# Kernel tuning notes

Hardware: AMD Instinct MI355X
Metric: run time of the kernel (lower is better)

The kernel has to match this reference:

```python
import jax, jax.numpy as jnp
import numpy as np

L, D, H, E, K, HID = 4096, 1024, 16, 8, 2, 4096
HEAD_DIM = D // H
SCALE = 1.0 / np.sqrt(HEAD_DIM)


def setup_inputs() -> dict:
    key = jax.random.key(0)
    ks = jax.random.split(key, 9)
    s = 0.02
    return {
        "Q": jax.random.normal(ks[0], (L, D), dtype=jnp.float32),
        "K": jax.random.normal(ks[1], (L, D), dtype=jnp.float32),
        "V": jax.random.normal(ks[2], (L, D), dtype=jnp.float32),
        "gate_w": jax.random.normal(ks[3], (D, E), dtype=jnp.float32) * s,
        "w1": jax.random.normal(ks[4], (E, D, HID), dtype=jnp.float32) * s,
        "b1": jnp.zeros((E, HID), dtype=jnp.float32),
        "w2": jax.random.normal(ks[5], (E, HID, D), dtype=jnp.float32) * s,
        "b2": jnp.zeros((E, D), dtype=jnp.float32),
    }


def attention(Q, Kt, V):
    # [L, D] -> [L, H, head_dim]
    q = Q.reshape(L, H, HEAD_DIM)
    k = Kt.reshape(L, H, HEAD_DIM)
    v = V.reshape(L, H, HEAD_DIM)
    scores = jnp.einsum("qhd,khd->hqk", q, k) * SCALE  # [H, L, L]
    probs = jax.nn.softmax(scores, axis=-1)
    out = jnp.einsum("hqk,khd->qhd", probs, v)  # [L, H, head_dim]
    return out.reshape(L, D)


def moe(x, gate_w, w1, b1, w2, b2):
    # x: [N, D]; top-k gating with softmax over selected logits
    logits = x @ gate_w  # [N, E]
    topv, topi = jax.lax.top_k(logits, K)  # [N, K]
    topw = jax.nn.softmax(topv, axis=-1)
    rows = jnp.arange(x.shape[0])[:, None]
    full_w = jnp.zeros_like(logits).at[rows, topi].set(topw)  # [N, E]
    # dense-masked expert compute (mathematically identical: zero weights kill
    # unrouted tokens). GELU is exact (erf), matching torch nn.GELU default.
    h = jax.nn.gelu(jnp.einsum("nd,edh->enh", x, w1) + b1[:, None, :],
                    approximate=False)  # [E, N, HID]
    y = jnp.einsum("enh,ehd->end", h, w2) + b2[:, None, :]  # [E, N, D]
    return jnp.einsum("ne,end->nd", full_w, y)  # weighted combine


def reference(Q, K, V, gate_w, w1, b1, w2, b2):
    attn_out = attention(Q, K, V)              # [L, D]
    out = moe(attn_out, gate_w, w1, b1, w2, b2)  # [L, D]
    return out
```

## Files before the change

kernel.cpp:

```cpp
#include <hip/hip_runtime.h>
#include <hip/hip_bf16.h>
#include <math.h>

#define L_SEQ 4096
#define DMODEL 1024
#define NHEAD 16
#define HDIM 64
#define NEXP 8
#define NHID 4096
#define NSLOT (L_SEQ * 2)

typedef __attribute__((ext_vector_type(4))) float f32x4;
typedef __attribute__((ext_vector_type(8))) short s16x8;
typedef __attribute__((ext_vector_type(4))) short s16x4;

__device__ __forceinline__ short f2bf(float f) {
  __hip_bfloat16 h = __float2bfloat16(f);
  return *reinterpret_cast<short*>(&h);
}
__device__ __forceinline__ float bf2f(short s) {
  __hip_bfloat16 h;
  *reinterpret_cast<short*>(&h) = s;
  return __bfloat162float(h);
}
__device__ __forceinline__ void split3(float a, short& h, short& m, short& l) {
  h = f2bf(a);
  float r = a - bf2f(h);
  m = f2bf(r);
  float r2 = r - bf2f(m);
  l = f2bf(r2);
}
__device__ __forceinline__ void tsplit3(float a, short& h, short& m, short& l) {
  unsigned u = __float_as_uint(a);
  unsigned uh = u & 0xffff0000u;
  float fh = __uint_as_float(uh);
  float r1 = a - fh;
  unsigned um = __float_as_uint(r1) & 0xffff0000u;
  float fm = __uint_as_float(um);
  float r2 = r1 - fm;
  unsigned ul = __float_as_uint(r2) & 0xffff0000u;
  h = (short)(uh >> 16); m = (short)(um >> 16); l = (short)(ul >> 16);
}
__device__ __forceinline__ void gload16(const void* g, void* l) {
  __builtin_amdgcn_global_load_lds(
      (const __attribute__((address_space(1))) void*)g,
      (__attribute__((address_space(3))) void*)l, 16, 0, 0);
}

__global__ __launch_bounds__(256) void split_kernel(const float* __restrict__ src,
                                                    short* __restrict__ hs,
                                                    short* __restrict__ ms,
                                                    short* __restrict__ ls,
                                                    float scale, int nquad) {
  int i = blockIdx.x * 256 + threadIdx.x;
  for (; i < nquad; i += gridDim.x * 256) {
    f32x4 a = reinterpret_cast<const f32x4*>(src)[i];
    a *= scale;
    s16x4 h4, m4, l4;
    #pragma unroll
    for (int j = 0; j < 4; ++j) {
      short h, m, l;
      split3(a[j], h, m, l);
      h4[j] = h; m4[j] = m; l4[j] = l;
    }
    reinterpret_cast<s16x4*>(hs)[i] = h4;
    reinterpret_cast<s16x4*>(ms)[i] = m4;
    reinterpret_cast<s16x4*>(ls)[i] = l4;
  }
}

__global__ __launch_bounds__(256) void split_vt_kernel(const float* __restrict__ V,
                                                       short* __restrict__ Vth,
                                                       short* __restrict__ Vtm,
                                                       short* __restrict__ Vtl) {
  __shared__ float Vlds[64][65];
  const int k0 = blockIdx.x * 64;
  const int head = blockIdx.y;
  const int t = threadIdx.x;
  {
    int r = t >> 2, c = (t & 3) * 16;
    const f32x4* src = reinterpret_cast<const f32x4*>(&V[(size_t)(k0 + r) * DMODEL + head * HDIM + c]);
    #pragma unroll
    for (int j = 0; j < 4; ++j)
      *reinterpret_cast<f32x4*>(&Vlds[r][c + 4 * j]) = src[j];
  }
  __syncthreads();
  {
    int d = t >> 2, kc = (t & 3) * 16;
    s16x8 h8[2], m8[2], l8[2];
    #pragma unroll
    for (int j = 0; j < 16; ++j) {
      float v = Vlds[kc + j][d];
      short h, m, l;
      split3(v, h, m, l);
      h8[j >> 3][j & 7] = h; m8[j >> 3][j & 7] = m; l8[j >> 3][j & 7] = l;
    }
    size_t base = (size_t)(head * HDIM + d) * L_SEQ + k0 + kc;
    *reinterpret_cast<s16x8*>(&Vth[base]) = h8[0];
    *reinterpret_cast<s16x8*>(&Vth[base + 8]) = h8[1];
    *reinterpret_cast<s16x8*>(&Vtm[base]) = m8[0];
    *reinterpret_cast<s16x8*>(&Vtm[base + 8]) = m8[1];
    *reinterpret_cast<s16x8*>(&Vtl[base]) = l8[0];
    *reinterpret_cast<s16x8*>(&Vtl[base + 8]) = l8[1];
  }
}

__global__ __launch_bounds__(256) void wtrans_kernel(const float* __restrict__ src,
                                                     short* __restrict__ dst,
                                                     int R, int C) {
  __shared__ float T[64][65];
  const int e = blockIdx.z;
  const int r0 = blockIdx.y * 64, c0 = blockIdx.x * 64;
  const size_t sbase = (size_t)e * R * C;
  const int t = threadIdx.x;
  {
    int rr = t >> 2, cc = (t & 3) * 16;
    #pragma unroll
    for (int j = 0; j < 4; ++j)
      *reinterpret_cast<f32x4*>(&T[rr][cc + 4 * j]) =
          *reinterpret_cast<const f32x4*>(&src[sbase + (size_t)(r0 + rr) * C + c0 + cc + 4 * j]);
  }
  __syncthreads();
  {
    int c = t >> 2, r = (t & 3) * 16;
    s16x8 v0, v1;
    #pragma unroll
    for (int j = 0; j < 8; ++j) { v0[j] = f2bf(T[r + j][c]); v1[j] = f2bf(T[r + 8 + j][c]); }
    size_t dbase = ((size_t)e * C + c0 + c) * R + r0 + r;
    *reinterpret_cast<s16x8*>(&dst[dbase]) = v0;
    *reinterpret_cast<s16x8*>(&dst[dbase + 8]) = v1;
  }
}

__global__ __launch_bounds__(256) void attn_mfma(
    const short* __restrict__ Qh, const short* __restrict__ Qm, const short* __restrict__ Ql,
    const short* __restrict__ Kh, const short* __restrict__ Km, const short* __restrict__ Kl,
    const short* __restrict__ Vth, const short* __restrict__ Vtm, const short* __restrict__ Vtl,
    float* __restrict__ X) {
  __shared__ short Ks[3][64][68];
  __shared__ short Vs[3][64][68];
  __shared__ short Ps[4][3][16][68];
  const int lin = blockIdx.x;
  const int swz = (lin & 7) * 128 + (lin >> 3);
  const int head = swz >> 6;
  const int q0 = (swz & 63) << 6;
  const int t = threadIdx.x;
  const int lane = t & 63;
  const int wq = t >> 6;
  const int lq = lane & 15;
  const int lg = lane >> 4;

  const short* Qp[3] = {Qh, Qm, Ql};
  const short* Kp[3] = {Kh, Km, Kl};
  const short* Vp[3] = {Vth, Vtm, Vtl};

  s16x8 qf[3][2];
  {
    size_t qrow = (size_t)(q0 + wq * 16 + lq) * DMODEL + head * HDIM;
    #pragma unroll
    for (int s = 0; s < 3; ++s)
      #pragma unroll
      for (int dc = 0; dc < 2; ++dc)
        qf[s][dc] = *reinterpret_cast<const s16x8*>(&Qp[s][qrow + dc * 32 + lg * 8]);
  }

  s16x8 sK[3][2], sV[3][2];
  const int c0 = t * 2;
  const int row0 = c0 >> 3, ch0 = (c0 & 7) * 8;
  const int row1 = (c0 + 1) >> 3, ch1 = ((c0 + 1) & 7) * 8;

  #define LOAD_TILE(k0v)                                                                  \
    _Pragma("unroll")                                                                     \
    for (int s = 0; s < 3; ++s) {                                                         \
      sK[s][0] = *reinterpret_cast<const s16x8*>(&Kp[s][(size_t)((k0v) + row0) * DMODEL + head * HDIM + ch0]); \
      sK[s][1] = *reinterpret_cast<const s16x8*>(&Kp[s][(size_t)((k0v) + row1) * DMODEL + head * HDIM + ch1]); \
      sV[s][0] = *reinterpret_cast<const s16x8*>(&Vp[s][(size_t)(head * HDIM + row0) * L_SEQ + (k0v) + ch0]);  \
      sV[s][1] = *reinterpret_cast<const s16x8*>(&Vp[s][(size_t)(head * HDIM + row1) * L_SEQ + (k0v) + ch1]);  \
    }

  f32x4 acc[4];
  #pragma unroll
  for (int dt = 0; dt < 4; ++dt) acc[dt] = (f32x4)0.f;
  float l_run = 0.f;
  const float LOG2E = 1.4426950408889634f;
  const float MBIAS = 46.166241f;

  LOAD_TILE(0);

  for (int kt64 = 0; kt64 < 64; ++kt64) {
    __syncthreads();
    #pragma unroll
    for (int s = 0; s < 3; ++s) {
      *reinterpret_cast<s16x8*>(&Ks[s][row0][ch0]) = sK[s][0];
      *reinterpret_cast<s16x8*>(&Ks[s][row1][ch1]) = sK[s][1];
      *reinterpret_cast<s16x8*>(&Vs[s][row0][ch0]) = sV[s][0];
      *reinterpret_cast<s16x8*>(&Vs[s][row1][ch1]) = sV[s][1];
    }
    __syncthreads();
    if (kt64 < 63) { LOAD_TILE((kt64 + 1) * 64); }

    f32x4 st[4];
    #pragma unroll
    for (int kt = 0; kt < 4; ++kt) {
      st[kt] = (f32x4)0.f;
      #pragma unroll
      for (int dc = 0; dc < 2; ++dc) {
        s16x8 ah = *reinterpret_cast<const s16x8*>(&Ks[0][kt * 16 + lq][dc * 32 + lg * 8]);
        s16x8 am = *reinterpret_cast<const s16x8*>(&Ks[1][kt * 16 + lq][dc * 32 + lg * 8]);
        s16x8 al = *reinterpret_cast<const s16x8*>(&Ks[2][kt * 16 + lq][dc * 32 + lg * 8]);
        st[kt] = __builtin_amdgcn_mfma_f32_16x16x32_bf16(am, qf[1][dc], st[kt], 0, 0, 0);
        st[kt] = __builtin_amdgcn_mfma_f32_16x16x32_bf16(al, qf[0][dc], st[kt], 0, 0, 0);
        st[kt] = __builtin_amdgcn_mfma_f32_16x16x32_bf16(ah, qf[2][dc], st[kt], 0, 0, 0);
        st[kt] = __builtin_amdgcn_mfma_f32_16x16x32_bf16(am, qf[0][dc], st[kt], 0, 0, 0);
        st[kt] = __builtin_amdgcn_mfma_f32_16x16x32_bf16(ah, qf[1][dc], st[kt], 0, 0, 0);
        st[kt] = __builtin_amdgcn_mfma_f32_16x16x32_bf16(ah, qf[0][dc], st[kt], 0, 0, 0);
      }
    }

    float psum = 0.f;
    #pragma unroll
    for (int kt = 0; kt < 4; ++kt) {
      s16x4 h4, m4, l4;
      #pragma unroll
      for (int r = 0; r < 4; ++r) {
        float p = exp2f(fmaf(st[kt][r], LOG2E, -MBIAS));
        psum += p;
        short h, m, l;
        tsplit3(p, h, m, l);
        h4[r] = h; m4[r] = m; l4[r] = l;
      }
      int kcol = kt * 16 + lg * 4;
      *reinterpret_cast<s16x4*>(&Ps[wq][0][lq][kcol]) = h4;
      *reinterpret_cast<s16x4*>(&Ps[wq][1][lq][kcol]) = m4;
      *reinterpret_cast<s16x4*>(&Ps[wq][2][lq][kcol]) = l4;
    }
    psum += __shfl_xor(psum, 16);
    psum += __shfl_xor(psum, 32);
    l_run += psum;

    #pragma unroll
    for (int kc = 0; kc < 2; ++kc) {
      s16x8 ph = *reinterpret_cast<const s16x8*>(&Ps[wq][0][lq][kc * 32 + lg * 8]);
      s16x8 pm = *reinterpret_cast<const s16x8*>(&Ps[wq][1][lq][kc * 32 + lg * 8]);
      s16x8 pl = *reinterpret_cast<const s16x8*>(&Ps[wq][2][lq][kc * 32 + lg * 8]);
      #pragma unroll
      for (int dt = 0; dt < 4; ++dt) {
        s16x8 vh = *reinterpret_cast<const s16x8*>(&Vs[0][dt * 16 + lq][kc * 32 + lg * 8]);
        s16x8 vm = *reinterpret_cast<const s16x8*>(&Vs[1][dt * 16 + lq][kc * 32 + lg * 8]);
        s16x8 vl = *reinterpret_cast<const s16x8*>(&Vs[2][dt * 16 + lq][kc * 32 + lg * 8]);
        acc[dt] = __builtin_amdgcn_mfma_f32_16x16x32_bf16(pm, vm, acc[dt], 0, 0, 0);
        acc[dt] = __builtin_amdgcn_mfma_f32_16x16x32_bf16(pl, vh, acc[dt], 0, 0, 0);
        acc[dt] = __builtin_amdgcn_mfma_f32_16x16x32_bf16(ph, vl, acc[dt], 0, 0, 0);
        acc[dt] = __builtin_amdgcn_mfma_f32_16x16x32_bf16(pm, vh, acc[dt], 0, 0, 0);
        acc[dt] = __builtin_amdgcn_mfma_f32_16x16x32_bf16(ph, vm, acc[dt], 0, 0, 0);
        acc[dt] = __builtin_amdgcn_mfma_f32_16x16x32_bf16(ph, vh, acc[dt], 0, 0, 0);
      }
    }
  }

  float inv = 1.f / l_run;
  float inv_r[4];
  #pragma unroll
  for (int r = 0; r < 4; ++r) {
    int src = (lg * 4 + r) << 2;
    inv_r[r] = __int_as_float(__builtin_amdgcn_ds_bpermute(src, __float_as_int(inv)));
  }
  #pragma unroll
  for (int dt = 0; dt < 4; ++dt)
    #pragma unroll
    for (int r = 0; r < 4; ++r)
      X[(size_t)(q0 + wq * 16 + lg * 4 + r) * DMODEL + head * HDIM + dt * 16 + lq] = acc[dt][r] * inv_r[r];
}

__global__ __launch_bounds__(256) void tobf16_kernel(const float* __restrict__ src,
                                                     short* __restrict__ dst, int n8) {
  int i = blockIdx.x * 256 + threadIdx.x;
  if (i >= n8) return;
  const f32x4* s = reinterpret_cast<const f32x4*>(src) + (size_t)i * 2;
  f32x4 a = s[0], b = s[1];
  s16x8 r;
  #pragma unroll
  for (int j = 0; j < 4; ++j) { r[j] = f2bf(a[j]); r[4 + j] = f2bf(b[j]); }
  reinterpret_cast<s16x8*>(dst)[i] = r;
}

__global__ __launch_bounds__(256) void gate_kernel(const float* __restrict__ X,
                                                   const float* __restrict__ GW,
                                                   int* __restrict__ tokE,
                                                   float* __restrict__ tokW,
                                                   int* __restrict__ meta) {
  const int gid = blockIdx.x * 256 + threadIdx.x;
  const int n = gid >> 6;
  const int lane = threadIdx.x & 63;
  double lacc[8];
  #pragma unroll
  for (int e = 0; e < 8; ++e) lacc[e] = 0.0;
  #pragma unroll
  for (int ch = 0; ch < 4; ++ch) {
    int d0 = ch * 256 + lane * 4;
    f32x4 xv = *reinterpret_cast<const f32x4*>(&X[(size_t)n * DMODEL + d0]);
    #pragma unroll
    for (int j = 0; j < 4; ++j) {
      const f32x4* g = reinterpret_cast<const f32x4*>(&GW[(size_t)(d0 + j) * 8]);
      f32x4 g0 = g[0], g1 = g[1];
      double xd = (double)xv[j];
      lacc[0] += xd * (double)g0[0]; lacc[1] += xd * (double)g0[1];
      lacc[2] += xd * (double)g0[2]; lacc[3] += xd * (double)g0[3];
      lacc[4] += xd * (double)g1[0]; lacc[5] += xd * (double)g1[1];
      lacc[6] += xd * (double)g1[2]; lacc[7] += xd * (double)g1[3];
    }
  }
  #pragma unroll
  for (int e = 0; e < 8; ++e) {
    double v = lacc[e];
    #pragma unroll
    for (int off = 32; off > 0; off >>= 1) v += __shfl_down(v, off);
    lacc[e] = v;
  }
  if (lane == 0) {
    float lg[8];
    #pragma unroll
    for (int e = 0; e < 8; ++e) lg[e] = (float)lacc[e];
    int i0 = 0;
    for (int e = 1; e < 8; ++e) if (lg[e] > lg[i0]) i0 = e;
    int i1 = -1;
    for (int e = 0; e < 8; ++e) {
      if (e == i0) continue;
      if (i1 < 0 || lg[e] > lg[i1]) i1 = e;
    }
    float eb = expf(lg[i1] - lg[i0]);
    float wa = 1.f / (1.f + eb);
    float wb = eb * wa;
    tokE[2 * n] = i0; tokE[2 * n + 1] = i1;
    tokW[2 * n] = wa; tokW[2 * n + 1] = wb;
    atomicAdd(&meta[i0], 1);
    atomicAdd(&meta[i1], 1);
  }
}

__global__ void scan_kernel(int* meta) {
  if (threadIdx.x == 0) {
    int s = 0;
    for (int e = 0; e < 8; ++e) { meta[8 + e] = s; meta[16 + e] = s; s += meta[e]; }
  }
}

__global__ __launch_bounds__(256) void assign_kernel(const int* __restrict__ tokE,
                                                     const float* __restrict__ tokW,
                                                     int* __restrict__ meta,
                                                     int* __restrict__ list,
                                                     float* __restrict__ wl) {
  int n = blockIdx.x * 256 + threadIdx.x;
  if (n >= L_SEQ) return;
  #pragma unroll
  for (int k2 = 0; k2 < 2; ++k2) {
    int e = tokE[2 * n + k2];
    int slot = atomicAdd(&meta[16 + e], 1);
    list[slot] = n;
    wl[slot] = tokW[2 * n + k2];
  }
}

__global__ __launch_bounds__(256) void gemm1p_kernel(const short* __restrict__ Xb,
                                                     const short* __restrict__ W1t,
                                                     const float* __restrict__ B1,
                                                     const int* __restrict__ meta,
                                                     const int* __restrict__ list,
                                                     short* __restrict__ Hb) {
  const int e = blockIdx.z;
  const int cntE = meta[e];
  const int lin = blockIdx.x + gridDim.x * blockIdx.y;
  const int nwg = gridDim.x * gridDim.y;
  const int swz = (lin & 7) * (nwg >> 3) + (lin >> 3);
  const int m0 = (swz % gridDim.x) << 7;
  const int n0 = (swz / gridDim.x) << 7;
  if (m0 >= cntE) return;
  const int baseE = meta[8 + e];

  __shared__ short As[2][128 * 64];
  __shared__ short Bs[2][128 * 64];

  const int t = threadIdx.x;
  const int l = t & 63;
  const int w = t >> 6;
  const int wm = w >> 1, wn = w & 1;
  const int ln = l & 15, kg = l >> 4;

  size_t asrc[4], bsrc[4];
  #pragma unroll
  for (int c = 0; c < 4; ++c) {
    int row = c * 32 + w * 8 + (l >> 3);
    int idx = m0 + row; if (idx > cntE - 1) idx = cntE - 1;
    int grow = list[baseE + idx];
    int sch = (l & 7) ^ (row & 7);
    asrc[c] = ((size_t)grow * DMODEL + sch * 8) * 2;
    bsrc[c] = (((size_t)e * NHID + n0 + row) * DMODEL + sch * 8) * 2;
  }

  f32x4 acc[4][4];
  #pragma unroll
  for (int mi = 0; mi < 4; ++mi)
    #pragma unroll
    for (int ni = 0; ni < 4; ++ni) acc[mi][ni] = (f32x4)0.f;

  #define STAGE1(buf, ktv) do {                                                     \
    size_t koff = (size_t)(ktv) * 128;                                              \
    _Pragma("unroll")                                                               \
    for (int c = 0; c < 4; ++c) {                                                   \
      gload16((const char*)Xb + asrc[c] + koff, (char*)As + (buf) * 16384 + c * 4096 + w * 1024);  \
      gload16((const char*)W1t + bsrc[c] + koff, (char*)Bs + (buf) * 16384 + c * 4096 + w * 1024); \
    } } while (0)

  STAGE1(0, 0);
  __syncthreads();
  int cur = 0;
  for (int kt = 0; kt < 16; ++kt) {
    if (kt < 15) STAGE1(cur ^ 1, kt + 1);
    #pragma unroll
    for (int dc = 0; dc < 2; ++dc) {
      s16x8 af[4];
      #pragma unroll
      for (int mi = 0; mi < 4; ++mi) {
        int row = wm * 64 + mi * 16 + ln;
        int c = (dc * 4 + kg) ^ (row & 7);
        af[mi] = *reinterpret_cast<const s16x8*>((char*)As + cur * 16384 + row * 128 + c * 16);
      }
      #pragma unroll
      for (int ni = 0; ni < 4; ++ni) {
        int col = wn * 64 + ni * 16 + ln;
        int c = (dc * 4 + kg) ^ (col & 7);
        s16x8 bfr = *reinterpret_cast<const s16x8*>((char*)Bs + cur * 16384 + col * 128 + c * 16);
        #pragma unroll
        for (int mi = 0; mi < 4; ++mi)
          acc[mi][ni] = __builtin_amdgcn_mfma_f32_16x16x32_bf16(af[mi], bfr, acc[mi][ni], 0, 0, 0);
      }
    }
    __syncthreads();
    cur ^= 1;
  }

  #pragma unroll
  for (int mi = 0; mi < 4; ++mi) {
    #pragma unroll
    for (int r = 0; r < 4; ++r) {
      int rl = wm * 64 + mi * 16 + kg * 4 + r;
      if (m0 + rl >= cntE) continue;
      size_t hrow = (size_t)(baseE + m0 + rl) * NHID;
      #pragma unroll
      for (int ni = 0; ni < 4; ++ni) {
        int col = n0 + wn * 64 + ni * 16 + ln;
        float z = acc[mi][ni][r] + B1[e * NHID + col];
        float g = 0.5f * z * (1.f + erff(z * 0.70710678118f));
        Hb[hrow + col] = f2bf(g);
      }
    }
  }
}

__global__ __launch_bounds__(256) void gemm2p_kernel(const short* __restrict__ Hb,
                                                     const short* __restrict__ W2t,
                                                     const float* __restrict__ B2,
                                                     const int* __restrict__ meta,
                                                     const int* __restrict__ list,
                                                     const float* __restrict__ wl,
                                                     float* __restrict__ out) {
  const int e = blockIdx.z;
  const int cntE = meta[e];
  const int lin = blockIdx.x + gridDim.x * blockIdx.y;
  const int nwg = gridDim.x * gridDim.y;
  const int swz = (lin & 7) * (nwg >> 3) + (lin >> 3);
  const int m0 = (swz % gridDim.x) << 7;
  const int n0 = (swz / gridDim.x) << 7;
  if (m0 >= cntE) return;
  const int baseE = meta[8 + e];

  __shared__ short As[2][128 * 64];
  __shared__ short Bs[2][128 * 64];

  const int t = threadIdx.x;
  const int l = t & 63;
  const int w = t >> 6;
  const int wm = w >> 1, wn = w & 1;
  const int ln = l & 15, kg = l >> 4;

  size_t asrc[4], bsrc[4];
  #pragma unroll
  for (int c = 0; c < 4; ++c) {
    int row = c * 32 + w * 8 + (l >> 3);
    int idx = m0 + row; if (idx > cntE - 1) idx = cntE - 1;
    int sch = (l & 7) ^ (row & 7);
    asrc[c] = (((size_t)(baseE + idx)) * NHID + sch * 8) * 2;
    bsrc[c] = (((size_t)e * DMODEL + n0 + row) * NHID + sch * 8) * 2;
  }

  f32x4 acc[4][4];
  #pragma unroll
  for (int mi = 0; mi < 4; ++mi)
    #pragma unroll
    for (int ni = 0; ni < 4; ++ni) acc[mi][ni] = (f32x4)0.f;

  #define STAGE2(buf, ktv) do {                                                     \
    size_t koff = (size_t)(ktv) * 128;                                              \
    _Pragma("unroll")                                                               \
    for (int c = 0; c < 4; ++c) {                                                   \
      gload16((const char*)Hb + asrc[c] + koff, (char*)As + (buf) * 16384 + c * 4096 + w * 1024);  \
      gload16((const char*)W2t + bsrc[c] + koff, (char*)Bs + (buf) * 16384 + c * 4096 + w * 1024); \
    } } while (0)

  STAGE2(0, 0);
  __syncthreads();
  int cur = 0;
  for (int kt = 0; kt < 64; ++kt) {
    if (kt < 63) STAGE2(cur ^ 1, kt + 1);
    #pragma unroll
    for (int dc = 0; dc < 2; ++dc) {
      s16x8 af[4];
      #pragma unroll
      for (int mi = 0; mi < 4; ++mi) {
        int row = wm * 64 + mi * 16 + ln;
        int c = (dc * 4 + kg) ^ (row & 7);
        af[mi] = *reinterpret_cast<const s16x8*>((char*)As + cur * 16384 + row * 128 + c * 16);
      }
      #pragma unroll
      for (int ni = 0; ni < 4; ++ni) {
        int col = wn * 64 + ni * 16 + ln;
        int c = (dc * 4 + kg) ^ (col & 7);
        s16x8 bfr = *reinterpret_cast<const s16x8*>((char*)Bs + cur * 16384 + col * 128 + c * 16);
        #pragma unroll
        for (int mi = 0; mi < 4; ++mi)
          acc[mi][ni] = __builtin_amdgcn_mfma_f32_16x16x32_bf16(af[mi], bfr, acc[mi][ni], 0, 0, 0);
      }
    }
    __syncthreads();
    cur ^= 1;
  }

  #pragma unroll
  for (int mi = 0; mi < 4; ++mi) {
    #pragma unroll
    for (int r = 0; r < 4; ++r) {
      int rl = wm * 64 + mi * 16 + kg * 4 + r;
      if (m0 + rl >= cntE) continue;
      int slot = baseE + m0 + rl;
      int token = list[slot];
      float wgt = wl[slot];
      #pragma unroll
      for (int ni = 0; ni < 4; ++ni) {
        int col = n0 + wn * 64 + ni * 16 + ln;
        float z = acc[mi][ni][r] + B2[e * DMODEL + col];
        atomicAdd(&out[(size_t)token * DMODEL + col], wgt * z);
      }
    }
  }
}

extern "C" void kernel_launch(void* const* d_in, const int* in_sizes, int n_in,
                              void* d_out, int out_size, void* d_ws, size_t ws_size,
                              hipStream_t stream) {
  const float* Q  = (const float*)d_in[0];
  const float* K  = (const float*)d_in[1];
  const float* V  = (const float*)d_in[2];
  const float* GW = (const float*)d_in[3];
  const float* W1 = (const float*)d_in[4];
  const float* B1 = (const float*)d_in[5];
  const float* W2 = (const float*)d_in[6];
  const float* B2 = (const float*)d_in[7];
  float* out = (float*)d_out;

  const size_t SPLIT = (size_t)L_SEQ * DMODEL;
  const size_t WT_BYTES = (size_t)NEXP * NHID * DMODEL * 2;
  const size_t SPLIT_REGION = SPLIT * 2 * 9;
  const size_t SMALL = (size_t)L_SEQ * 2 * 4 * 2 + (size_t)NSLOT * 4 * 2 + 256;
  const size_t PRIMARY_BYTES = WT_BYTES * 2 + SPLIT_REGION + SPLIT * 4 + SMALL;
  if (ws_size < PRIMARY_BYTES) return;

  char* ws = (char*)d_ws;
  const int nquad = (int)(SPLIT / 4);

  size_t off = 0;
  short* W1t = (short*)(ws + off); off += WT_BYTES;
  short* W2t = (short*)(ws + off); off += WT_BYTES;
  char*  splits = ws + off;        off += SPLIT_REGION;
  short* Qh = (short*)(splits);
  short* Qm = Qh + SPLIT;  short* Ql = Qm + SPLIT;
  short* Kh = Ql + SPLIT;  short* Km = Kh + SPLIT;  short* Kl = Km + SPLIT;
  short* Vth = Kl + SPLIT; short* Vtm = Vth + SPLIT; short* Vtl = Vtm + SPLIT;
  short* Hb = (short*)splits;
  short* Xb = (short*)(splits + (size_t)NSLOT * NHID * 2);
  float* Xf = (float*)(ws + off);  off += SPLIT * 4;
  int*   tokE = (int*)(ws + off);  off += (size_t)L_SEQ * 2 * 4;
  float* tokW = (float*)(ws + off); off += (size_t)L_SEQ * 2 * 4;
  int*   list = (int*)(ws + off);  off += (size_t)NSLOT * 4;
  float* wl = (float*)(ws + off);  off += (size_t)NSLOT * 4;
  int*   meta = (int*)(ws + off);  off += 256;

  hipMemsetAsync(out, 0, (size_t)out_size * sizeof(float), stream);
  hipMemsetAsync(meta, 0, 256, stream);

  wtrans_kernel<<<dim3(64, 16, 8), 256, 0, stream>>>(W1, W1t, DMODEL, NHID);
  wtrans_kernel<<<dim3(16, 64, 8), 256, 0, stream>>>(W2, W2t, NHID, DMODEL);
  split_kernel<<<dim3(2048), 256, 0, stream>>>(Q, Qh, Qm, Ql, 0.125f, nquad);
  split_kernel<<<dim3(2048), 256, 0, stream>>>(K, Kh, Km, Kl, 1.0f, nquad);
  split_vt_kernel<<<dim3(64, 16), 256, 0, stream>>>(V, Vth, Vtm, Vtl);
  attn_mfma<<<dim3(1024), 256, 0, stream>>>(Qh, Qm, Ql, Kh, Km, Kl, Vth, Vtm, Vtl, Xf);
  tobf16_kernel<<<dim3(2048), 256, 0, stream>>>(Xf, Xb, (int)(SPLIT / 8));
  gate_kernel<<<dim3(1024), 256, 0, stream>>>(Xf, GW, tokE, tokW, meta);
  scan_kernel<<<1, 64, 0, stream>>>(meta);
  assign_kernel<<<dim3(16), 256, 0, stream>>>(tokE, tokW, meta, list, wl);
  gemm1p_kernel<<<dim3(32, 32, 8), 256, 0, stream>>>(Xb, W1t, B1, meta, list, Hb);
  gemm2p_kernel<<<dim3(32, 8, 8), 256, 0, stream>>>(Hb, W2t, B2, meta, list, wl, out);
}
```

Before: 1.099 ms.

## Deepen software pipelining in attention and MoE GEMM kernels

The attention kernel now uses 32-key tiles in double-buffered LDS, with register-staged prefetch two tiles ahead and compute interleaved between the two buffers. Both expert GEMM kernels move from a 2-stage 64-wide K pipeline to a 4-buffer 32-wide K pipeline that keeps three loads in flight, using explicit vmcnt waits and a single raw barrier per step. The aim is to hide global-load latency behind MFMA work and cut barrier overhead. In exchange, the K-steps are smaller, which adds loop and wait overhead, and the hand-coded vmcnt counts must match the real number of issued loads.

After: 1.144 ms. 4.1% more time.

```diff
diff --git a/kernel.cpp b/kernel.cpp
--- a/kernel.cpp
+++ b/kernel.cpp
@@ -137,9 +137,9 @@
     const short* __restrict__ Kh, const short* __restrict__ Km, const short* __restrict__ Kl,
     const short* __restrict__ Vth, const short* __restrict__ Vtm, const short* __restrict__ Vtl,
     float* __restrict__ X) {
-  __shared__ short Ks[3][64][68];
-  __shared__ short Vs[3][64][68];
-  __shared__ short Ps[4][3][16][68];
+  __shared__ short Ks[2][3][32][68];
+  __shared__ short Vs[2][3][64][36];
+  __shared__ short Ps[4][3][16][36];
   const int lin = blockIdx.x;
   const int swz = (lin & 7) * 128 + (lin >> 3);
   const int head = swz >> 6;
@@ -164,19 +164,22 @@
         qf[s][dc] = *reinterpret_cast<const s16x8*>(&Qp[s][qrow + dc * 32 + lg * 8]);
   }
 
-  s16x8 sK[3][2], sV[3][2];
-  const int c0 = t * 2;
-  const int row0 = c0 >> 3, ch0 = (c0 & 7) * 8;
-  const int row1 = (c0 + 1) >> 3, ch1 = ((c0 + 1) & 7) * 8;
-
-  #define LOAD_TILE(k0v)                                                                  \
-    _Pragma("unroll")                                                                     \
-    for (int s = 0; s < 3; ++s) {                                                         \
-      sK[s][0] = *reinterpret_cast<const s16x8*>(&Kp[s][(size_t)((k0v) + row0) * DMODEL + head * HDIM + ch0]); \
-      sK[s][1] = *reinterpret_cast<const s16x8*>(&Kp[s][(size_t)((k0v) + row1) * DMODEL + head * HDIM + ch1]); \
-      sV[s][0] = *reinterpret_cast<const s16x8*>(&Vp[s][(size_t)(head * HDIM + row0) * L_SEQ + (k0v) + ch0]);  \
-      sV[s][1] = *reinterpret_cast<const s16x8*>(&Vp[s][(size_t)(head * HDIM + row1) * L_SEQ + (k0v) + ch1]);  \
-    }
+  const int krow = t >> 3, kch = (t & 7) * 8;
+  const int vrow = t >> 2, vch = (t & 3) * 8;
+
+  s16x8 rK0[3], rV0[3], rK1[3], rV1[3];
+
+  #define ALOAD(RK, RV, tile) do { int k0_ = (tile) * 32;                                   \
+    _Pragma("unroll") for (int s = 0; s < 3; ++s) {                                         \
+      RK[s] = *reinterpret_cast<const s16x8*>(&Kp[s][(size_t)(k0_ + krow) * DMODEL + head * HDIM + kch]); \
+      RV[s] = *reinterpret_cast<const s16x8*>(&Vp[s][(size_t)(head * HDIM + vrow) * L_SEQ + k0_ + vch]);  \
+    } } while (0)
+
+  #define AWRITE(RK, RV, BF) do {                                                           \
+    _Pragma("unroll") for (int s = 0; s < 3; ++s) {                                         \
+      *reinterpret_cast<s16x8*>(&Ks[BF][s][krow][kch]) = RK[s];                             \
+      *reinterpret_cast<s16x8*>(&Vs[BF][s][vrow][vch]) = RV[s];                             \
+    } } while (0)
 
   f32x4 acc[4];
   #pragma unroll
@@ -185,77 +188,76 @@
   const float LOG2E = 1.4426950408889634f;
   const float MBIAS = 46.166241f;
 
-  LOAD_TILE(0);
-
-  for (int kt64 = 0; kt64 < 64; ++kt64) {
+  #define ACOMPUTE(BF) do {                                                                 \
+    f32x4 st0 = (f32x4)0.f, st1 = (f32x4)0.f;                                               \
+    _Pragma("unroll") for (int dc = 0; dc < 2; ++dc) {                                      \
+      s16x8 ah = *reinterpret_cast<const s16x8*>(&Ks[BF][0][lq][dc * 32 + lg * 8]);         \
+      s16x8 am = *reinterpret_cast<const s16x8*>(&Ks[BF][1][lq][dc * 32 + lg * 8]);         \
+      s16x8 al = *reinterpret_cast<const s16x8*>(&Ks[BF][2][lq][dc * 32 + lg * 8]);         \
+      st0 = __builtin_amdgcn_mfma_f32_16x16x32_bf16(am, qf[1][dc], st0, 0, 0, 0);           \
+      st0 = __builtin_amdgcn_mfma_f32_16x16x32_bf16(al, qf[0][dc], st0, 0, 0, 0);           \
+      st0 = __builtin_amdgcn_mfma_f32_16x16x32_bf16(ah, qf[2][dc], st0, 0, 0, 0);           \
+      st0 = __builtin_amdgcn_mfma_f32_16x16x32_bf16(am, qf[0][dc], st0, 0, 0, 0);           \
+      st0 = __builtin_amdgcn_mfma_f32_16x16x32_bf16(ah, qf[1][dc], st0, 0, 0, 0);           \
+      st0 = __builtin_amdgcn_mfma_f32_16x16x32_bf16(ah, qf[0][dc], st0, 0, 0, 0);           \
+      s16x8 bh = *reinterpret_cast<const s16x8*>(&Ks[BF][0][16 + lq][dc * 32 + lg * 8]);    \
+      s16x8 bm = *reinterpret_cast<const s16x8*>(&Ks[BF][1][16 + lq][dc * 32 + lg * 8]);    \
+      s16x8 bl = *reinterpret_cast<const s16x8*>(&Ks[BF][2][16 + lq][dc * 32 + lg * 8]);    \
+      st1 = __builtin_amdgcn_mfma_f32_16x16x32_bf16(bm, qf[1][dc], st1, 0, 0, 0);           \
+      st1 = __builtin_amdgcn_mfma_f32_16x16x32_bf16(bl, qf[0][dc], st1, 0, 0, 0);           \
+      st1 = __builtin_amdgcn_mfma_f32_16x16x32_bf16(bh, qf[2][dc], st1, 0, 0, 0);           \
+      st1 = __builtin_amdgcn_mfma_f32_16x16x32_bf16(bm, qf[0][dc], st1, 0, 0, 0);           \
+      st1 = __builtin_amdgcn_mfma_f32_16x16x32_bf16(bh, qf[1][dc], st1, 0, 0, 0);           \
+      st1 = __builtin_amdgcn_mfma_f32_16x16x32_bf16(bh, qf[0][dc], st1, 0, 0, 0);           \
+    }                                                                                        \
+    float psum = 0.f;                                                                        \
+    { s16x4 h4, m4, l4;                                                                      \
+      _Pragma("unroll") for (int r = 0; r < 4; ++r) {                                        \
+        float p = exp2f(fmaf(st0[r], LOG2E, -MBIAS)); psum += p;                             \
+        short h_, m_, l_; tsplit3(p, h_, m_, l_); h4[r] = h_; m4[r] = m_; l4[r] = l_; }      \
+      *reinterpret_cast<s16x4*>(&Ps[wq][0][lq][lg * 4]) = h4;                                \
+      *reinterpret_cast<s16x4*>(&Ps[wq][1][lq][lg * 4]) = m4;                                \
+      *reinterpret_cast<s16x4*>(&Ps[wq][2][lq][lg * 4]) = l4; }                              \
+    { s16x4 h4, m4, l4;                                                                      \
+      _Pragma("unroll") for (int r = 0; r < 4; ++r) {                                        \
+        float p = exp2f(fmaf(st1[r], LOG2E, -MBIAS)); psum += p;                             \
+        short h_, m_, l_; tsplit3(p, h_, m_, l_); h4[r] = h_; m4[r] = m_; l4[r] = l_; }      \
+      *reinterpret_cast<s16x4*>(&Ps[wq][0][lq][16 + lg * 4]) = h4;                           \
+      *reinterpret_cast<s16x4*>(&Ps[wq][1][lq][16 + lg * 4]) = m4;                           \
+      *reinterpret_cast<s16x4*>(&Ps[wq][2][lq][16 + lg * 4]) = l4; }                         \
+    psum += __shfl_xor(psum, 16);                                                            \
+    psum += __shfl_xor(psum, 32);                                                            \
+    l_run += psum;                                                                           \
+    s16x8 ph = *reinterpret_cast<const s16x8*>(&Ps[wq][0][lq][lg * 8]);                      \
+    s16x8 pm = *reinterpret_cast<const s16x8*>(&Ps[wq][1][lq][lg * 8]);                      \
+    s16x8 pl = *reinterpret_cast<const s16x8*>(&Ps[wq][2][lq][lg * 8]);                      \
+    _Pragma("unroll") for (int dt = 0; dt < 4; ++dt) {                                       \
+      s16x8 vh = *reinterpret_cast<const s16x8*>(&Vs[BF][0][dt * 16 + lq][lg * 8]);          \
+      s16x8 vm = *reinterpret_cast<const s16x8*>(&Vs[BF][1][dt * 16 + lq][lg * 8]);          \
+      s16x8 vl = *reinterpret_cast<const s16x8*>(&Vs[BF][2][dt * 16 + lq][lg * 8]);          \
+      acc[dt] = __builtin_amdgcn_mfma_f32_16x16x32_bf16(pm, vm, acc[dt], 0, 0, 0);           \
+      acc[dt] = __builtin_amdgcn_mfma_f32_16x16x32_bf16(pl, vh, acc[dt], 0, 0, 0);           \
+      acc[dt] = __builtin_amdgcn_mfma_f32_16x16x32_bf16(ph, vl, acc[dt], 0, 0, 0);           \
+      acc[dt] = __builtin_amdgcn_mfma_f32_16x16x32_bf16(pm, vh, acc[dt], 0, 0, 0);           \
+      acc[dt] = __builtin_amdgcn_mfma_f32_16x16x32_bf16(ph, vm, acc[dt], 0, 0, 0);           \
+      acc[dt] = __builtin_amdgcn_mfma_f32_16x16x32_bf16(ph, vh, acc[dt], 0, 0, 0);           \
+    } } while (0)
+
+  ALOAD(rK0, rV0, 0);
+  ALOAD(rK1, rV1, 1);
+  AWRITE(rK0, rV0, 0);
+
+  for (int tp = 0; tp < 64; ++tp) {
     __syncthreads();
-    #pragma unroll
-    for (int s = 0; s < 3; ++s) {
-      *reinterpret_cast<s16x8*>(&Ks[s][row0][ch0]) = sK[s][0];
-      *reinterpret_cast<s16x8*>(&Ks[s][row1][ch1]) = sK[s][1];
-      *reinterpret_cast<s16x8*>(&Vs[s][row0][ch0]) = sV[s][0];
-      *reinterpret_cast<s16x8*>(&Vs[s][row1][ch1]) = sV[s][1];
-    }
+    if (tp < 63) ALOAD(rK0, rV0, 2 * tp + 2);
+    ACOMPUTE(0);
+    AWRITE(rK1, rV1, 1);
     __syncthreads();
-    if (kt64 < 63) { LOAD_TILE((kt64 + 1) * 64); }
-
-    f32x4 st[4];
-    #pragma unroll
-    for (int kt = 0; kt < 4; ++kt) {
-      st[kt] = (f32x4)0.f;
-      #pragma unroll
-      for (int dc = 0; dc < 2; ++dc) {
-        s16x8 ah = *reinterpret_cast<const s16x8*>(&Ks[0][kt * 16 + lq][dc * 32 + lg * 8]);
-        s16x8 am = *reinterpret_cast<const s16x8*>(&Ks[1][kt * 16 + lq][dc * 32 + lg * 8]);
-        s16x8 al = *reinterpret_cast<const s16x8*>(&Ks[2][kt * 16 + lq][dc * 32 + lg * 8]);
-        st[kt] = __builtin_amdgcn_mfma_f32_16x16x32_bf16(am, qf[1][dc], st[kt], 0, 0, 0);
-        st[kt] = __builtin_amdgcn_mfma_f32_16x16x32_bf16(al, qf[0][dc], st[kt], 0, 0, 0);
-        st[kt] = __builtin_amdgcn_mfma_f32_16x16x32_bf16(ah, qf[2][dc], st[kt], 0, 0, 0);
-        st[kt] = __builtin_amdgcn_mfma_f32_16x16x32_bf16(am, qf[0][dc], st[kt], 0, 0, 0);
-        st[kt] = __builtin_amdgcn_mfma_f32_16x16x32_bf16(ah, qf[1][dc], st[kt], 0, 0, 0);
-        st[kt] = __builtin_amdgcn_mfma_f32_16x16x32_bf16(ah, qf[0][dc], st[kt], 0, 0, 0);
-      }
-    }
-
-    float psum = 0.f;
-    #pragma unroll
-    for (int kt = 0; kt < 4; ++kt) {
-      s16x4 h4, m4, l4;
-      #pragma unroll
-      for (int r = 0; r < 4; ++r) {
-        float p = exp2f(fmaf(st[kt][r], LOG2E, -MBIAS));
-        psum += p;
-        short h, m, l;
-        tsplit3(p, h, m, l);
-        h4[r] = h; m4[r] = m; l4[r] = l;
-      }
-      int kcol = kt * 16 + lg * 4;
-      *reinterpret_cast<s16x4*>(&Ps[wq][0][lq][kcol]) = h4;
-      *reinterpret_cast<s16x4*>(&Ps[wq][1][lq][kcol]) = m4;
-      *reinterpret_cast<s16x4*>(&Ps[wq][2][lq][kcol]) = l4;
-    }
-    psum += __shfl_xor(psum, 16);
-    psum += __shfl_xor(psum, 32);
-    l_run += psum;
-
-    #pragma unroll
-    for (int kc = 0; kc < 2; ++kc) {
-      s16x8 ph = *reinterpret_cast<const s16x8*>(&Ps[wq][0][lq][kc * 32 + lg * 8]);
-      s16x8 pm = *reinterpret_cast<const s16x8*>(&Ps[wq][1][lq][kc * 32 + lg * 8]);
-      s16x8 pl = *reinterpret_cast<const s16x8*>(&Ps[wq][2][lq][kc * 32 + lg * 8]);
-      #pragma unroll
-      for (int dt = 0; dt < 4; ++dt) {
-        s16x8 vh = *reinterpret_cast<const s16x8*>(&Vs[0][dt * 16 + lq][kc * 32 + lg * 8]);
-        s16x8 vm = *reinterpret_cast<const s16x8*>(&Vs[1][dt * 16 + lq][kc * 32 + lg * 8]);
-        s16x8 vl = *reinterpret_cast<const s16x8*>(&Vs[2][dt * 16 + lq][kc * 32 + lg * 8]);
-        acc[dt] = __builtin_amdgcn_mfma_f32_16x16x32_bf16(pm, vm, acc[dt], 0, 0, 0);
-        acc[dt] = __builtin_amdgcn_mfma_f32_16x16x32_bf16(pl, vh, acc[dt], 0, 0, 0);
-        acc[dt] = __builtin_amdgcn_mfma_f32_16x16x32_bf16(ph, vl, acc[dt], 0, 0, 0);
-        acc[dt] = __builtin_amdgcn_mfma_f32_16x16x32_bf16(pm, vh, acc[dt], 0, 0, 0);
-        acc[dt] = __builtin_amdgcn_mfma_f32_16x16x32_bf16(ph, vm, acc[dt], 0, 0, 0);
-        acc[dt] = __builtin_amdgcn_mfma_f32_16x16x32_bf16(ph, vh, acc[dt], 0, 0, 0);
-      }
-    }
+    if (tp < 63) {
+      ALOAD(rK1, rV1, 2 * tp + 3);
+    }
+    ACOMPUTE(1);
+    if (tp < 63) AWRITE(rK0, rV0, 0);
   }
 
   float inv = 1.f / l_run;
@@ -377,8 +379,8 @@
   if (m0 >= cntE) return;
   const int baseE = meta[8 + e];
 
-  __shared__ short As[2][128 * 64];
-  __shared__ short Bs[2][128 * 64];
+  __shared__ short As[4][128 * 32];
+  __shared__ short Bs[4][128 * 32];
 
   const int t = threadIdx.x;
   const int l = t & 63;
@@ -386,13 +388,13 @@
   const int wm = w >> 1, wn = w & 1;
   const int ln = l & 15, kg = l >> 4;
 
-  size_t asrc[4], bsrc[4];
-  #pragma unroll
-  for (int c = 0; c < 4; ++c) {
-    int row = c * 32 + w * 8 + (l >> 3);
+  size_t asrc[2], bsrc[2];
+  #pragma unroll
+  for (int c = 0; c < 2; ++c) {
+    int row = c * 64 + w * 16 + (l >> 2);
     int idx = m0 + row; if (idx > cntE - 1) idx = cntE - 1;
     int grow = list[baseE + idx];
-    int sch = (l & 7) ^ (row & 7);
+    int sch = (l & 3) ^ (row & 3);
     asrc[c] = ((size_t)grow * DMODEL + sch * 8) * 2;
     bsrc[c] = (((size_t)e * NHID + n0 + row) * DMODEL + sch * 8) * 2;
   }
@@ -403,40 +405,40 @@
     #pragma unroll
     for (int ni = 0; ni < 4; ++ni) acc[mi][ni] = (f32x4)0.f;
 
-  #define STAGE1(buf, ktv) do {                                                     \
-    size_t koff = (size_t)(ktv) * 128;                                              \
-    _Pragma("unroll")                                                               \
-    for (int c = 0; c < 4; ++c) {                                                   \
-      gload16((const char*)Xb + asrc[c] + koff, (char*)As + (buf) * 16384 + c * 4096 + w * 1024);  \
-      gload16((const char*)W1t + bsrc[c] + koff, (char*)Bs + (buf) * 16384 + c * 4096 + w * 1024); \
+  #define STG1(h_) do { int bf_ = (h_) & 3; size_t ko_ = (size_t)(h_) * 64;                 \
+    _Pragma("unroll") for (int c_ = 0; c_ < 2; ++c_) {                                      \
+      gload16((const char*)Xb + asrc[c_] + ko_, (char*)As + bf_ * 8192 + c_ * 4096 + w * 1024);  \
+      gload16((const char*)W1t + bsrc[c_] + ko_, (char*)Bs + bf_ * 8192 + c_ * 4096 + w * 1024); \
     } } while (0)
 
-  STAGE1(0, 0);
-  __syncthreads();
-  int cur = 0;
-  for (int kt = 0; kt < 16; ++kt) {
-    if (kt < 15) STAGE1(cur ^ 1, kt + 1);
-    #pragma unroll
-    for (int dc = 0; dc < 2; ++dc) {
-      s16x8 af[4];
+  const int H = DMODEL / 32;
+  STG1(0); STG1(1); STG1(2);
+  for (int h = 0; h < H; ++h) {
+    int rem = H - 1 - h;
+    if (rem >= 2)      asm volatile("s_waitcnt vmcnt(8)" ::: "memory");
+    else if (rem == 1) asm volatile("s_waitcnt vmcnt(4)" ::: "memory");
+    else               asm volatile("s_waitcnt vmcnt(0)" ::: "memory");
+    __builtin_amdgcn_s_barrier();
+    __builtin_amdgcn_sched_barrier(0);
+    if (h + 3 < H) STG1(h + 3);
+    const char* abase = (const char*)As + (h & 3) * 8192;
+    const char* bbase = (const char*)Bs + (h & 3) * 8192;
+    s16x8 af[4];
+    #pragma unroll
+    for (int mi = 0; mi < 4; ++mi) {
+      int row = wm * 64 + mi * 16 + ln;
+      int cc = kg ^ (row & 3);
+      af[mi] = *reinterpret_cast<const s16x8*>(abase + row * 64 + cc * 16);
+    }
+    #pragma unroll
+    for (int ni = 0; ni < 4; ++ni) {
+      int col = wn * 64 + ni * 16 + ln;
+      int cc = kg ^ (col & 3);
+      s16x8 bfr = *reinterpret_cast<const s16x8*>(bbase + col * 64 + cc * 16);
       #pragma unroll
-      for (int mi = 0; mi < 4; ++mi) {
-        int row = wm * 64 + mi * 16 + ln;
-        int c = (dc * 4 + kg) ^ (row & 7);
-        af[mi] = *reinterpret_cast<const s16x8*>((char*)As + cur * 16384 + row * 128 + c * 16);
-      }
-      #pragma unroll
-      for (int ni = 0; ni < 4; ++ni) {
-        int col = wn * 64 + ni * 16 + ln;
-        int c = (dc * 4 + kg) ^ (col & 7);
-        s16x8 bfr = *reinterpret_cast<const s16x8*>((char*)Bs + cur * 16384 + col * 128 + c * 16);
-        #pragma unroll
-        for (int mi = 0; mi < 4; ++mi)
-          acc[mi][ni] = __builtin_amdgcn_mfma_f32_16x16x32_bf16(af[mi], bfr, acc[mi][ni], 0, 0, 0);
-      }
-    }
-    __syncthreads();
-    cur ^= 1;
+      for (int mi = 0; mi < 4; ++mi)
+        acc[mi][ni] = __builtin_amdgcn_mfma_f32_16x16x32_bf16(af[mi], bfr, acc[mi][ni], 0, 0, 0);
+    }
   }
 
   #pragma unroll
@@ -474,8 +476,8 @@
   if (m0 >= cntE) return;
   const int baseE = meta[8 + e];
 
-  __shared__ short As[2][128 * 64];
-  __shared__ short Bs[2][128 * 64];
+  __shared__ short As[4][128 * 32];
+  __shared__ short Bs[4][128 * 32];
 
   const int t = threadIdx.x;
   const int l = t & 63;
@@ -483,12 +485,12 @@
   const int wm = w >> 1, wn = w & 1;
   const int ln = l & 15, kg = l >> 4;
 
-  size_t asrc[4], bsrc[4];
-  #pragma unroll
-  for (int c = 0; c < 4; ++c) {
-    int row = c * 32 + w * 8 + (l >> 3);
+  size_t asrc[2], bsrc[2];
+  #pragma unroll
+  for (int c = 0; c < 2; ++c) {
+    int row = c * 64 + w * 16 + (l >> 2);
     int idx = m0 + row; if (idx > cntE - 1) idx = cntE - 1;
-    int sch = (l & 7) ^ (row & 7);
+    int sch = (l & 3) ^ (row & 3);
     asrc[c] = (((size_t)(baseE + idx)) * NHID + sch * 8) * 2;
     bsrc[c] = (((size_t)e * DMODEL + n0 + row) * NHID + sch * 8) * 2;
   }
@@ -499,40 +501,40 @@
     #pragma unroll
     for (int ni = 0; ni < 4; ++ni) acc[mi][ni] = (f32x4)0.f;
 
-  #define STAGE2(buf, ktv) do {                                                     \
-    size_t koff = (size_t)(ktv) * 128;                                              \
-    _Pragma("unroll")                                                               \
-    for (int c = 0; c < 4; ++c) {                                                   \
-      gload16((const char*)Hb + asrc[c] + koff, (char*)As + (buf) * 16384 + c * 4096 + w * 1024);  \
-      gload16((const char*)W2t + bsrc[c] + koff, (char*)Bs + (buf) * 16384 + c * 4096 + w * 1024); \
+  #define STG2(h_) do { int bf_ = (h_) & 3; size_t ko_ = (size_t)(h_) * 64;                 \
+    _Pragma("unroll") for (int c_ = 0; c_ < 2; ++c_) {                                      \
+      gload16((const char*)Hb + asrc[c_] + ko_, (char*)As + bf_ * 8192 + c_ * 4096 + w * 1024);  \
+      gload16((const char*)W2t + bsrc[c_] + ko_, (char*)Bs + bf_ * 8192 + c_ * 4096 + w * 1024); \
     } } while (0)
 
-  STAGE2(0, 0);
-  __syncthreads();
-  int cur = 0;
-  for (int kt = 0; kt < 64; ++kt) {
-    if (kt < 63) STAGE2(cur ^ 1, kt + 1);
-    #pragma unroll
-    for (int dc = 0; dc < 2; ++dc) {
-      s16x8 af[4];
+  const int H = NHID / 32;
+  STG2(0); STG2(1); STG2(2);
+  for (int h = 0; h < H; ++h) {
+    int rem = H - 1 - h;
+    if (rem >= 2)      asm volatile("s_waitcnt vmcnt(8)" ::: "memory");
+    else if (rem == 1) asm volatile("s_waitcnt vmcnt(4)" ::: "memory");
+    else               asm volatile("s_waitcnt vmcnt(0)" ::: "memory");
+    __builtin_amdgcn_s_barrier();
+    __builtin_amdgcn_sched_barrier(0);
+    if (h + 3 < H) STG2(h + 3);
+    const char* abase = (const char*)As + (h & 3) * 8192;
+    const char* bbase = (const char*)Bs + (h & 3) * 8192;
+    s16x8 af[4];
+    #pragma unroll
+    for (int mi = 0; mi < 4; ++mi) {
+      int row = wm * 64 + mi * 16 + ln;
+      int cc = kg ^ (row & 3);
+      af[mi] = *reinterpret_cast<const s16x8*>(abase + row * 64 + cc * 16);
+    }
+    #pragma unroll
+    for (int ni = 0; ni < 4; ++ni) {
+      int col = wn * 64 + ni * 16 + ln;
+      int cc = kg ^ (col & 3);
+      s16x8 bfr = *reinterpret_cast<const s16x8*>(bbase + col * 64 + cc * 16);
       #pragma unroll
-      for (int mi = 0; mi < 4; ++mi) {
-        int row = wm * 64 + mi * 16 + ln;
-        int c = (dc * 4 + kg) ^ (row & 7);
-        af[mi] = *reinterpret_cast<const s16x8*>((char*)As + cur * 16384 + row * 128 + c * 16);
-      }
-      #pragma unroll
-      for (int ni = 0; ni < 4; ++ni) {
-        int col = wn * 64 + ni * 16 + ln;
-        int c = (dc * 4 + kg) ^ (col & 7);
-        s16x8 bfr = *reinterpret_cast<const s16x8*>((char*)Bs + cur * 16384 + col * 128 + c * 16);
-        #pragma unroll
-        for (int mi = 0; mi < 4; ++mi)
-          acc[mi][ni] = __builtin_amdgcn_mfma_f32_16x16x32_bf16(af[mi], bfr, acc[mi][ni], 0, 0, 0);
-      }
-    }
-    __syncthreads();
-    cur ^= 1;
+      for (int mi = 0; mi < 4; ++mi)
+        acc[mi][ni] = __builtin_amdgcn_mfma_f32_16x16x32_bf16(af[mi], bfr, acc[mi][ni], 0, 0, 0);
+    }
   }
 
   #pragma unroll
```
